# Performance work log

Hardware: AMD Instinct MI355X
Metric: run time of the kernel (lower is better)

Reference implementation:

```python
import jax, jax.numpy as jnp
import numpy as np

# Constants mirroring the torch module / argparse defaults
DECAY = 0.2           # LIF membrane decay
DECAY_TRACE = 0.99    # pre-synaptic trace decay
DECAY_TRACE2 = 0.99   # post-synaptic trace decay
INH = 1.625           # lateral inhibition strength (mode='max')
A1 = 0.96             # STDP potentiation coefficient
A2 = 0.53             # STDP depression coefficient
PLUS = 0.002          # adaptive threshold increment
THR_CAP = 350.0       # threshold cap in getthresh
B, IN, OUT = 128, 8192, 4096


def setup_inputs() -> dict:
    key = jax.random.key(0)
    ks = jax.random.split(key, 7)
    x = (jax.random.uniform(ks[0], (B, IN)) < 0.1).astype(jnp.float32)
    # weight after normweight(): clamp to [0,1], scale each row so row-max == 0.1
    w = jax.random.uniform(ks[1], (OUT, IN))
    w = jnp.clip(w, 0.0, 1.0)
    w = w / (w.max(axis=1, keepdims=True) / 0.1)
    mem = jax.random.uniform(ks[2], (B, OUT)) * 10.0          # warm membrane state
    threshold = 20.0 + 40.0 * jax.random.uniform(ks[3], (OUT,))  # per-neuron adaptive threshold
    trace = jax.random.uniform(ks[4], (B, IN))                 # warm pre-trace
    trace2 = jax.random.uniform(ks[5], (B, OUT))               # warm post-trace
    wta_rand = jax.random.uniform(ks[6], (B, OUT))             # WTA random tie-breaker
    return {"x": x, "weight": w, "mem": mem, "threshold": threshold,
            "trace": trace, "trace2": trace2, "wta_rand": wta_rand,
            "time_window": 10}


def reference(x, weight, mem, threshold, trace, trace2, wta_rand, time_window):
    batch = x.shape[0]
    # linear (no bias): i = x @ W^T   [B, OUT]
    i = x @ weight.T
    # --- LIF membrane update with hard reset ---
    mem = mem * DECAY + i
    s = (mem >= threshold[None, :]).astype(x.dtype)
    mem = mem * (1.0 - s)
    # --- winner-take-all (k=1) with random tie-break among spiking neurons ---
    pos = s * wta_rand
    winner = s * (pos >= pos.max(axis=1, keepdims=True)).astype(x.dtype)
    # --- adaptive lateral inhibition (mode='max'): suppress losers' membrane ---
    any_spk = winner.max(axis=1, keepdims=True)  # rows that fired
    mem = mem - INH * i.max(axis=1, keepdims=True) * (1.0 - winner) * any_spk
    spikes = winner
    # --- STDP traces and weight updates (training path) ---
    trace2_dec = trace2 * DECAY_TRACE2               # trace2 BEFORE adding current spikes
    dw2 = jnp.einsum('bo,bi->oi', trace2_dec, x)     # post-pre depression term
    trace_new = trace * DECAY_TRACE + x              # pre-trace replaces x for dw
    dw = jnp.einsum('bo,bi->oi', spikes, trace_new)  # pre-post potentiation term
    # --- adaptive threshold balance (ATB) ---
    thr = threshold + PLUS * (i * spikes).sum(0)
    thr = thr - jnp.maximum(thr.max() - THR_CAP, 0.0)
    # accumulated STDP weight change self.dw
    dw_total = (A1 * dw - A2 * dw2) / (time_window * batch)
    return spikes, dw_total, thr, mem
```

## Files before the change

### kernel.cpp

```cpp
#include <hip/hip_runtime.h>
#include <hip/hip_bf16.h>

typedef unsigned short u16;
typedef __bf16 bf16x8 __attribute__((ext_vector_type(8)));
typedef u16   u16x4  __attribute__((ext_vector_type(4)));
typedef u16   u16x8  __attribute__((ext_vector_type(8)));
typedef float f32x4  __attribute__((ext_vector_type(4)));

#define MFMA16(A,B,C) __builtin_amdgcn_mfma_f32_16x16x32_bf16(A,B,C,0,0,0)

#define B_DIM   128
#define IN_DIM  8192
#define OUT_DIM 4096

__device__ __forceinline__ u16 f2bf(float f){
  __hip_bfloat16 h = __float2bfloat16(f);
  return __builtin_bit_cast(u16, h);
}
__device__ __forceinline__ float bf2f(u16 u){
  __hip_bfloat16 h = __builtin_bit_cast(__hip_bfloat16, u);
  return __bfloat162float(h);
}

__global__ __launch_bounds__(256) void prep(const float* __restrict__ x,
    const float* __restrict__ trace, const float* __restrict__ trace2,
    const int* __restrict__ twp, u16* __restrict__ xbf,
    u16* __restrict__ Bcat, u16* __restrict__ Acat){
  __shared__ u16 s0[64*130];
  __shared__ u16 s1[64*130];
  const int tid = threadIdx.x;
  if (blockIdx.x < 128){
    const int in0 = blockIdx.x*64;
    #pragma unroll
    for (int rep=0; rep<8; ++rep){
      int flat = rep*256 + tid;
      int b = flat >> 4, i4 = (flat & 15)*4;
      size_t gi = (size_t)b*IN_DIM + in0 + i4;
      float4 xv = *reinterpret_cast<const float4*>(&x[gi]);
      float4 tv = *reinterpret_cast<const float4*>(&trace[gi]);
      u16 xb[4];
      #pragma unroll
      for (int e=0;e<4;++e){
        float xe = (&xv.x)[e];
        xb[e] = f2bf(xe);
        s0[(i4+e)*130 + b] = xb[e];
        s1[(i4+e)*130 + b] = f2bf(__fadd_rn(__fmul_rn(0.99f, (&tv.x)[e]), xe));
      }
      *reinterpret_cast<u16x4*>(&xbf[gi]) = (u16x4){xb[0],xb[1],xb[2],xb[3]};
    }
    __syncthreads();
    #pragma unroll
    for (int rep=0; rep<32; ++rep){
      int flat = rep*256 + tid;
      int row = flat >> 7, bc = flat & 127;
      size_t base = (size_t)(in0+row)*256;
      Bcat[base + bc]       = s1[row*130 + bc];
      Bcat[base + 128 + bc] = s0[row*130 + bc];
    }
  } else {
    const int o0 = (blockIdx.x - 128)*64;
    const float scale = -(0.53f*0.99f) / (float)(twp[0]*B_DIM);
    #pragma unroll
    for (int rep=0; rep<8; ++rep){
      int flat = rep*256 + tid;
      int b = flat >> 4, o4 = (flat & 15)*4;
      float4 v = *reinterpret_cast<const float4*>(&trace2[(size_t)b*OUT_DIM + o0 + o4]);
      #pragma unroll
      for (int e=0;e<4;++e) s0[(o4+e)*130 + b] = f2bf((&v.x)[e]*scale);
    }
    __syncthreads();
    #pragma unroll
    for (int rep=0; rep<32; ++rep){
      int flat = rep*256 + tid;
      int row = flat >> 7, bc = flat & 127;
      Acat[(size_t)(o0+row)*256 + 128 + bc] = s0[row*130 + bc];
    }
  }
}

__global__ __launch_bounds__(256) void t128s(const float* __restrict__ spikes,
    const int* __restrict__ twp, u16* __restrict__ Acat){
  __shared__ u16 s0[64*130];
  const int o0 = blockIdx.x*64;
  const int tid = threadIdx.x;
  const float scale = 0.96f / (float)(twp[0]*B_DIM);
  #pragma unroll
  for (int rep=0; rep<8; ++rep){
    int flat = rep*256 + tid;
    int b = flat >> 4, o4 = (flat & 15)*4;
    float4 v = *reinterpret_cast<const float4*>(&spikes[(size_t)b*OUT_DIM + o0 + o4]);
    #pragma unroll
    for (int e=0;e<4;++e) s0[(o4+e)*130 + b] = f2bf((&v.x)[e]*scale);
  }
  __syncthreads();
  #pragma unroll
  for (int rep=0; rep<32; ++rep){
    int flat = rep*256 + tid;
    int row = flat >> 7, bc = flat & 127;
    Acat[(size_t)(o0+row)*256 + bc] = s0[row*130 + bc];
  }
}

__global__ __launch_bounds__(256) void k1_gemm(const float* __restrict__ W,
    const u16* __restrict__ xbf, float* __restrict__ part){
  const int m0    = blockIdx.x*32;
  const int kc    = blockIdx.z;
  const int kbase = kc*1024;
  const int tid   = threadIdx.x;
  const int lane  = tid & 63, wid = tid >> 6;
  const int n0    = blockIdx.y*128 + wid*32;
  const int l15   = lane & 15, lg = lane >> 4;

  f32x4 acc[2][2];
  #pragma unroll
  for (int a=0;a<2;++a)
    #pragma unroll
    for (int c=0;c<2;++c){ acc[a][c][0]=0.f; acc[a][c][1]=0.f; acc[a][c][2]=0.f; acc[a][c][3]=0.f; }

  const u16*   a0 = &xbf[(size_t)(m0 + l15)*IN_DIM + kbase + 8*lg];
  const u16*   a1 = &xbf[(size_t)(m0 + 16 + l15)*IN_DIM + kbase + 8*lg];
  const float* w0 = &W[(size_t)(n0 + l15)*IN_DIM + kbase + 8*lg];
  const float* w1 = &W[(size_t)(n0 + 16 + l15)*IN_DIM + kbase + 8*lg];

  #pragma unroll 2
  for (int s=0; s<32; ++s){
    const int k = s*32;
    bf16x8 af[2];
    af[0] = *reinterpret_cast<const bf16x8*>(a0 + k);
    af[1] = *reinterpret_cast<const bf16x8*>(a1 + k);
    #pragma unroll
    for (int ni=0; ni<2; ++ni){
      const float* wp = (ni ? w1 : w0) + k;
      float4 wa = *reinterpret_cast<const float4*>(wp);
      float4 wb = *reinterpret_cast<const float4*>(wp + 4);
      u16 h[8], l[8];
      #pragma unroll
      for (int e=0;e<4;++e){
        float c0 = (&wa.x)[e];
        u16 hh = f2bf(c0);
        h[e] = hh; l[e] = f2bf(__fsub_rn(c0, bf2f(hh)));
        float c1 = (&wb.x)[e];
        u16 hh1 = f2bf(c1);
        h[4+e] = hh1; l[4+e] = f2bf(__fsub_rn(c1, bf2f(hh1)));
      }
      bf16x8 bh = __builtin_bit_cast(bf16x8, (u16x8){h[0],h[1],h[2],h[3],h[4],h[5],h[6],h[7]});
      bf16x8 bl = __builtin_bit_cast(bf16x8, (u16x8){l[0],l[1],l[2],l[3],l[4],l[5],l[6],l[7]});
      acc[0][ni] = MFMA16(af[0], bh, acc[0][ni]);
      acc[1][ni] = MFMA16(af[1], bh, acc[1][ni]);
      acc[0][ni] = MFMA16(af[0], bl, acc[0][ni]);
      acc[1][ni] = MFMA16(af[1], bl, acc[1][ni]);
    }
  }
  #pragma unroll
  for (int mi=0;mi<2;++mi)
    #pragma unroll
    for (int ni=0;ni<2;++ni)
      #pragma unroll
      for (int r=0;r<4;++r){
        int row = m0 + 16*mi + 4*lg + r;
        int col = n0 + 16*ni + l15;
        part[((size_t)kc*B_DIM + row)*OUT_DIM + col] = acc[mi][ni][r];
      }
}

__global__ __launch_bounds__(256) void k2a(const float* __restrict__ part,
    const float* __restrict__ mem, const float* __restrict__ thr,
    const float* __restrict__ wta, float* __restrict__ iacc,
    float* __restrict__ vbuf, float* __restrict__ pbuf,
    float* __restrict__ cm){
  const int b  = blockIdx.x;
  const int ch = blockIdx.y;
  const int o  = ch*1024 + threadIdx.x*4;
  const size_t base = (size_t)b*OUT_DIM;

  f32x4 a = *reinterpret_cast<const f32x4*>(&part[base + o]);
  #pragma unroll
  for (int c=1;c<8;++c){
    f32x4 p4 = *reinterpret_cast<const f32x4*>(&part[((size_t)c*B_DIM + b)*OUT_DIM + o]);
    #pragma unroll
    for (int e=0;e<4;++e) a[e] = __fadd_rn(a[e], p4[e]);
  }
  *reinterpret_cast<f32x4*>(&iacc[base + o]) = a;

  f32x4 m4 = *reinterpret_cast<const f32x4*>(&mem[base + o]);
  f32x4 t4 = *reinterpret_cast<const f32x4*>(&thr[o]);
  f32x4 w4 = *reinterpret_cast<const f32x4*>(&wta[base + o]);
  f32x4 v4, p4e;
  float pmax = -3.4e38f, imax = -3.4e38f, anyv = 0.f;
  #pragma unroll
  for (int e=0;e<4;++e){
    float ii = a[e];
    float v  = __fadd_rn(__fmul_rn(m4[e], 0.2f), ii);
    bool  s  = (v >= t4[e]);
    v4[e]  = v;
    p4e[e] = s ? w4[e] : -1.0f;
    pmax = fmaxf(pmax, p4e[e]);
    imax = fmaxf(imax, ii);
    if (s) anyv = 1.f;
  }
  *reinterpret_cast<f32x4*>(&vbuf[base + o]) = v4;
  *reinterpret_cast<f32x4*>(&pbuf[base + o]) = p4e;

  #pragma unroll
  for (int off=32; off>=1; off>>=1){
    pmax = fmaxf(pmax, __shfl_xor(pmax, off));
    imax = fmaxf(imax, __shfl_xor(imax, off));
    anyv = fmaxf(anyv, __shfl_xor(anyv, off));
  }
  __shared__ float sp[4], si[4], sa[4];
  const int wid = threadIdx.x>>6, lane = threadIdx.x&63;
  if (lane==0){ sp[wid]=pmax; si[wid]=imax; sa[wid]=anyv; }
  __syncthreads();
  if (threadIdx.x==0){
    float pm = fmaxf(fmaxf(sp[0],sp[1]), fmaxf(sp[2],sp[3]));
    float im = fmaxf(fmaxf(si[0],si[1]), fmaxf(si[2],si[3]));
    float an = fmaxf(fmaxf(sa[0],sa[1]), fmaxf(sa[2],sa[3]));
    cm[(size_t)(b*4 + ch)*4 + 0] = pm;
    cm[(size_t)(b*4 + ch)*4 + 1] = im;
    cm[(size_t)(b*4 + ch)*4 + 2] = an;
  }
}

__global__ __launch_bounds__(256) void k2b(const float* __restrict__ vbuf,
    const float* __restrict__ pbuf, const float* __restrict__ cm,
    float* __restrict__ spikes, float* __restrict__ mem_out){
  const int b  = blockIdx.x;
  const int ch = blockIdx.y;
  const int o  = ch*1024 + threadIdx.x*4;
  const size_t base = (size_t)b*OUT_DIM;

  float pmax = -3.4e38f, imax = -3.4e38f, anyv = 0.f;
  #pragma unroll
  for (int c2=0;c2<4;++c2){
    pmax = fmaxf(pmax, cm[(size_t)(b*4 + c2)*4 + 0]);
    imax = fmaxf(imax, cm[(size_t)(b*4 + c2)*4 + 1]);
    anyv = fmaxf(anyv, cm[(size_t)(b*4 + c2)*4 + 2]);
  }
  const float isub = __fmul_rn(1.625f, imax);

  f32x4 v4 = *reinterpret_cast<const f32x4*>(&vbuf[base + o]);
  f32x4 p4 = *reinterpret_cast<const f32x4*>(&pbuf[base + o]);
  f32x4 sp4, mm4;
  #pragma unroll
  for (int e=0;e<4;++e){
    bool s   = (p4[e] >= 0.f);
    bool win = s && (p4[e] >= pmax);
    sp4[e] = win ? 1.f : 0.f;
    float mv  = s ? 0.f : v4[e];
    float sub = (anyv>0.f && !win) ? isub : 0.f;
    mm4[e] = __fsub_rn(mv, sub);
  }
  *reinterpret_cast<f32x4*>(&spikes[base + o])  = sp4;
  *reinterpret_cast<f32x4*>(&mem_out[base + o]) = mm4;
}

__global__ __launch_bounds__(256) void k3a(const float* __restrict__ iacc,
    const float* __restrict__ spikes, float* __restrict__ thrpart){
  const int o  = blockIdx.x*256 + threadIdx.x;
  const int bc = blockIdx.y;
  float acc = 0.f;
  #pragma unroll
  for (int bb=0; bb<16; ++bb){
    int b = bc*16 + bb;
    acc = __fadd_rn(acc, __fmul_rn(iacc[(size_t)b*OUT_DIM+o], spikes[(size_t)b*OUT_DIM+o]));
  }
  thrpart[(size_t)bc*OUT_DIM + o] = acc;
}

__global__ __launch_bounds__(1024) void k3bc(const float* __restrict__ thrpart,
    const float* __restrict__ threshold, float* __restrict__ thr_out){
  const int tid = threadIdx.x;
  const int o = tid*4;
  f32x4 s = *reinterpret_cast<const f32x4*>(&thrpart[o]);
  #pragma unroll
  for (int c=1;c<8;++c){
    f32x4 p4 = *reinterpret_cast<const f32x4*>(&thrpart[(size_t)c*OUT_DIM + o]);
    #pragma unroll
    for (int e=0;e<4;++e) s[e] = __fadd_rn(s[e], p4[e]);
  }
  f32x4 t4 = *reinterpret_cast<const f32x4*>(&threshold[o]);
  float t0[4];
  #pragma unroll
  for (int e=0;e<4;++e) t0[e] = __fadd_rn(t4[e], __fmul_rn(0.002f, s[e]));
  float m = fmaxf(fmaxf(t0[0],t0[1]), fmaxf(t0[2],t0[3]));
  #pragma unroll
  for (int off=32; off>=1; off>>=1) m = fmaxf(m, __shfl_xor(m, off));
  __shared__ float sm16[16];
  const int wid = tid>>6, lane = tid&63;
  if (lane==0) sm16[wid] = m;
  __syncthreads();
  float g = sm16[0];
  #pragma unroll
  for (int k=1;k<16;++k) g = fmaxf(g, sm16[k]);
  float ex = fmaxf(__fsub_rn(g, 350.f), 0.f);
  f32x4 outv;
  #pragma unroll
  for (int e=0;e<4;++e) outv[e] = __fsub_rn(t0[e], ex);
  *reinterpret_cast<f32x4*>(&thr_out[o]) = outv;
}

__global__ __launch_bounds__(256) void k4_dw(const u16* __restrict__ Acat,
    const u16* __restrict__ Bcat, float* __restrict__ dw){
  const int ot = blockIdx.x;
  const int it = blockIdx.y;
  const int tid = threadIdx.x;
  const int lane = tid&63, wid = tid>>6;
  const int l15 = lane&15, lg = lane>>4;
  const int o0 = ot*64;
  const int iw = it*256 + wid*64;
  f32x4 acc[4][4];
  #pragma unroll
  for (int a=0;a<4;++a)
    #pragma unroll
    for (int c=0;c<4;++c){ acc[a][c][0]=0.f; acc[a][c][1]=0.f; acc[a][c][2]=0.f; acc[a][c][3]=0.f; }

  const size_t abase = (size_t)(o0 + l15)*256 + 8*lg;
  const size_t bbase = (size_t)(iw + l15)*256 + 8*lg;
  #pragma unroll
  for (int ks=0; ks<8; ++ks){
    const int k = ks*32;
    bf16x8 a[4], bb[4];
    #pragma unroll
    for (int mi=0;mi<4;++mi)
      a[mi] = *reinterpret_cast<const bf16x8*>(&Acat[abase + (size_t)mi*16*256 + k]);
    #pragma unroll
    for (int ni=0;ni<4;++ni)
      bb[ni] = *reinterpret_cast<const bf16x8*>(&Bcat[bbase + (size_t)ni*16*256 + k]);
    #pragma unroll
    for (int mi=0;mi<4;++mi)
      #pragma unroll
      for (int ni=0;ni<4;++ni)
        acc[mi][ni] = MFMA16(a[mi], bb[ni], acc[mi][ni]);
  }
  #pragma unroll
  for (int mi=0;mi<4;++mi)
    #pragma unroll
    for (int ni=0;ni<4;++ni)
      #pragma unroll
      for (int r=0;r<4;++r)
        dw[(size_t)(o0 + 16*mi + 4*lg + r)*IN_DIM + iw + 16*ni + l15] = acc[mi][ni][r];
}

extern "C" void kernel_launch(void* const* d_in, const int* in_sizes, int n_in,
                              void* d_out, int out_size, void* d_ws, size_t ws_size,
                              hipStream_t stream) {
  (void)in_sizes; (void)n_in; (void)out_size; (void)ws_size;
  const float* x      = (const float*)d_in[0];
  const float* weight = (const float*)d_in[1];
  const float* mem    = (const float*)d_in[2];
  const float* thresh = (const float*)d_in[3];
  const float* trace  = (const float*)d_in[4];
  const float* trace2 = (const float*)d_in[5];
  const float* wta    = (const float*)d_in[6];
  const int*   twp    = (const int*)d_in[7];

  float* out    = (float*)d_out;
  float* spikes = out;
  float* dwout  = out + 524288;
  float* throut = out + 34078720;
  float* memout = out + 34082816;

  char* ws = (char*)d_ws;
  float* iacc    = (float*)ws;
  u16*   xbf     = (u16*)(ws + (2u<<20));
  u16*   Acat    = (u16*)(ws + (4u<<20));
  u16*   Bcat    = (u16*)(ws + (6u<<20));
  float* thrpart = (float*)(ws + (10u<<20));
  float* cm      = (float*)(ws + (10u<<20) + (256u<<10));
  float* vbuf    = (float*)(ws + (12u<<20));
  float* pbuf    = (float*)(ws + (14u<<20));

  float* part = dwout;

  prep  <<<dim3(192),     dim3(256),  0, stream>>>(x, trace, trace2, twp, xbf, Bcat, Acat);
  k1_gemm<<<dim3(4,32,8), dim3(256),  0, stream>>>(weight, xbf, part);
  k2a   <<<dim3(128,4),   dim3(256),  0, stream>>>(part, mem, thresh, wta, iacc, vbuf, pbuf, cm);
  k2b   <<<dim3(128,4),   dim3(256),  0, stream>>>(vbuf, pbuf, cm, spikes, memout);
  t128s <<<dim3(64),      dim3(256),  0, stream>>>(spikes, twp, Acat);
  k3a   <<<dim3(16,8),    dim3(256),  0, stream>>>(iacc, spikes, thrpart);
  k3bc  <<<dim3(1),       dim3(1024), 0, stream>>>(thrpart, thresh, throut);
  k4_dw <<<dim3(64,32),   dim3(256),  0, stream>>>(Acat, Bcat, dwout);
}
```

Measured before the change: 382.2 us.

## Retile k1 GEMM so each block covers all batch rows, converting weights once

The first GEMM is retiled so each wave owns 16 output columns across all 128 batch rows. Each fp32 weight element is then loaded and split into bf16 hi/lo only once, where before it was reloaded and reconverted by 4 separate M-blocks. The next weight chunk is also software-prefetched into registers while the current one is converted and fed to the MFMAs. The cost is 8 accumulator tiles per wave, more x loads per step, and a grid cut from 1024 to 512 blocks.

```diff
diff --git a/kernel.cpp b/kernel.cpp
--- a/kernel.cpp
+++ b/kernel.cpp
@@ -103,64 +103,58 @@
 
 __global__ __launch_bounds__(256) void k1_gemm(const float* __restrict__ W,
     const u16* __restrict__ xbf, float* __restrict__ part){
-  const int m0    = blockIdx.x*32;
-  const int kc    = blockIdx.z;
+  const int kc    = blockIdx.y;
   const int kbase = kc*1024;
   const int tid   = threadIdx.x;
   const int lane  = tid & 63, wid = tid >> 6;
-  const int n0    = blockIdx.y*128 + wid*32;
+  const int n0    = blockIdx.x*64 + wid*16;
   const int l15   = lane & 15, lg = lane >> 4;
 
-  f32x4 acc[2][2];
-  #pragma unroll
-  for (int a=0;a<2;++a)
-    #pragma unroll
-    for (int c=0;c<2;++c){ acc[a][c][0]=0.f; acc[a][c][1]=0.f; acc[a][c][2]=0.f; acc[a][c][3]=0.f; }
-
-  const u16*   a0 = &xbf[(size_t)(m0 + l15)*IN_DIM + kbase + 8*lg];
-  const u16*   a1 = &xbf[(size_t)(m0 + 16 + l15)*IN_DIM + kbase + 8*lg];
-  const float* w0 = &W[(size_t)(n0 + l15)*IN_DIM + kbase + 8*lg];
-  const float* w1 = &W[(size_t)(n0 + 16 + l15)*IN_DIM + kbase + 8*lg];
-
-  #pragma unroll 2
+  f32x4 acc[8];
+  #pragma unroll
+  for (int mi=0;mi<8;++mi){ acc[mi][0]=0.f; acc[mi][1]=0.f; acc[mi][2]=0.f; acc[mi][3]=0.f; }
+
+  const u16*   ap = &xbf[(size_t)l15*IN_DIM + kbase + 8*lg];
+  const float* wp = &W[(size_t)(n0 + l15)*IN_DIM + kbase + 8*lg];
+
+  float4 wa = *reinterpret_cast<const float4*>(wp);
+  float4 wb = *reinterpret_cast<const float4*>(wp + 4);
+
   for (int s=0; s<32; ++s){
     const int k = s*32;
-    bf16x8 af[2];
-    af[0] = *reinterpret_cast<const bf16x8*>(a0 + k);
-    af[1] = *reinterpret_cast<const bf16x8*>(a1 + k);
-    #pragma unroll
-    for (int ni=0; ni<2; ++ni){
-      const float* wp = (ni ? w1 : w0) + k;
-      float4 wa = *reinterpret_cast<const float4*>(wp);
-      float4 wb = *reinterpret_cast<const float4*>(wp + 4);
-      u16 h[8], l[8];
-      #pragma unroll
-      for (int e=0;e<4;++e){
-        float c0 = (&wa.x)[e];
-        u16 hh = f2bf(c0);
-        h[e] = hh; l[e] = f2bf(__fsub_rn(c0, bf2f(hh)));
-        float c1 = (&wb.x)[e];
-        u16 hh1 = f2bf(c1);
-        h[4+e] = hh1; l[4+e] = f2bf(__fsub_rn(c1, bf2f(hh1)));
-      }
-      bf16x8 bh = __builtin_bit_cast(bf16x8, (u16x8){h[0],h[1],h[2],h[3],h[4],h[5],h[6],h[7]});
-      bf16x8 bl = __builtin_bit_cast(bf16x8, (u16x8){l[0],l[1],l[2],l[3],l[4],l[5],l[6],l[7]});
-      acc[0][ni] = MFMA16(af[0], bh, acc[0][ni]);
-      acc[1][ni] = MFMA16(af[1], bh, acc[1][ni]);
-      acc[0][ni] = MFMA16(af[0], bl, acc[0][ni]);
-      acc[1][ni] = MFMA16(af[1], bl, acc[1][ni]);
-    }
-  }
-  #pragma unroll
-  for (int mi=0;mi<2;++mi)
-    #pragma unroll
-    for (int ni=0;ni<2;++ni)
-      #pragma unroll
-      for (int r=0;r<4;++r){
-        int row = m0 + 16*mi + 4*lg + r;
-        int col = n0 + 16*ni + l15;
-        part[((size_t)kc*B_DIM + row)*OUT_DIM + col] = acc[mi][ni][r];
-      }
+    float4 na, nb;
+    if (s < 31){
+      na = *reinterpret_cast<const float4*>(wp + k + 32);
+      nb = *reinterpret_cast<const float4*>(wp + k + 36);
+    }
+    u16 h[8], l[8];
+    #pragma unroll
+    for (int e=0;e<4;++e){
+      float c0 = (&wa.x)[e];
+      u16 hh = f2bf(c0);
+      h[e] = hh; l[e] = f2bf(__fsub_rn(c0, bf2f(hh)));
+      float c1 = (&wb.x)[e];
+      u16 hh1 = f2bf(c1);
+      h[4+e] = hh1; l[4+e] = f2bf(__fsub_rn(c1, bf2f(hh1)));
+    }
+    bf16x8 bh = __builtin_bit_cast(bf16x8, (u16x8){h[0],h[1],h[2],h[3],h[4],h[5],h[6],h[7]});
+    bf16x8 bl = __builtin_bit_cast(bf16x8, (u16x8){l[0],l[1],l[2],l[3],l[4],l[5],l[6],l[7]});
+    #pragma unroll
+    for (int mi=0;mi<8;++mi){
+      bf16x8 af = *reinterpret_cast<const bf16x8*>(ap + (size_t)mi*16*IN_DIM + k);
+      acc[mi] = MFMA16(af, bh, acc[mi]);
+      acc[mi] = MFMA16(af, bl, acc[mi]);
+    }
+    wa = na; wb = nb;
+  }
+  #pragma unroll
+  for (int mi=0;mi<8;++mi)
+    #pragma unroll
+    for (int r=0;r<4;++r){
+      int row = 16*mi + 4*lg + r;
+      int col = n0 + l15;
+      part[((size_t)kc*B_DIM + row)*OUT_DIM + col] = acc[mi][r];
+    }
 }
 
 __global__ __launch_bounds__(256) void k2a(const float* __restrict__ part,
@@ -372,12 +366,12 @@
 
   float* part = dwout;
 
-  prep  <<<dim3(192),     dim3(256),  0, stream>>>(x, trace, trace2, twp, xbf, Bcat, Acat);
-  k1_gemm<<<dim3(4,32,8), dim3(256),  0, stream>>>(weight, xbf, part);
-  k2a   <<<dim3(128,4),   dim3(256),  0, stream>>>(part, mem, thresh, wta, iacc, vbuf, pbuf, cm);
-  k2b   <<<dim3(128,4),   dim3(256),  0, stream>>>(vbuf, pbuf, cm, spikes, memout);
-  t128s <<<dim3(64),      dim3(256),  0, stream>>>(spikes, twp, Acat);
-  k3a   <<<dim3(16,8),    dim3(256),  0, stream>>>(iacc, spikes, thrpart);
-  k3bc  <<<dim3(1),       dim3(1024), 0, stream>>>(thrpart, thresh, throut);
-  k4_dw <<<dim3(64,32),   dim3(256),  0, stream>>>(Acat, Bcat, dwout);
-}
+  prep  <<<dim3(192),    dim3(256),  0, stream>>>(x, trace, trace2, twp, xbf, Bcat, Acat);
+  k1_gemm<<<dim3(64,8),  dim3(256),  0, stream>>>(weight, xbf, part);
+  k2a   <<<dim3(128,4),  dim3(256),  0, stream>>>(part, mem, thresh, wta, iacc, vbuf, pbuf, cm);
+  k2b   <<<dim3(128,4),  dim3(256),  0, stream>>>(vbuf, pbuf, cm, spikes, memout);
+  t128s <<<dim3(64),     dim3(256),  0, stream>>>(spikes, twp, Acat);
+  k3a   <<<dim3(16,8),   dim3(256),  0, stream>>>(iacc, spikes, thrpart);
+  k3bc  <<<dim3(1),      dim3(1024), 0, stream>>>(thrpart, thresh, throut);
+  k4_dw <<<dim3(64,32),  dim3(256),  0, stream>>>(Acat, Bcat, dwout);
+}
```

Result: no change. 388.1 us (+1.6%).
